# Kernel tuning notes

Hardware: AMD Instinct MI355X
Metric: run time of the kernel (lower is better)

## Reference

```python
import jax, jax.numpy as jnp
import numpy as np

N, E = 100000, 1600000
IN_C, HID, OUT_C, EDGE_D, GRAPH_D = 32, 32, 8, 16, 16

def _lin_w(key, fan_in, fan_out):
    return jax.random.normal(key, (fan_in, fan_out), dtype=jnp.float32) * (1.0 / np.sqrt(fan_in))

def setup_inputs() -> dict:
    key = jax.random.key(0)
    ks = jax.random.split(key, 12)
    return {
        "x": jax.random.uniform(ks[0], (N, IN_C), dtype=jnp.float32),
        "edge_attr": jax.random.uniform(ks[1], (E, EDGE_D), dtype=jnp.float32),
        "graph_attr": jax.random.uniform(ks[2], (1, GRAPH_D), dtype=jnp.float32),
        "edge_index": jax.random.randint(ks[3], (2, E), 0, N, dtype=jnp.int32),
        "batch": jnp.zeros((N,), dtype=jnp.int32),
        "W_node": _lin_w(ks[4], IN_C, HID),
        "b_node": jnp.zeros((HID,), jnp.float32),
        "W_graph": _lin_w(ks[5], GRAPH_D, GRAPH_D),
        "b_graph": jnp.zeros((GRAPH_D,), jnp.float32),
        "W_edge_agg": _lin_w(ks[6], 2 * HID + EDGE_D + GRAPH_D, EDGE_D),
        "b_edge_agg": jnp.zeros((EDGE_D,), jnp.float32),
        "W_node_agg": _lin_w(ks[7], EDGE_D + HID + GRAPH_D, HID),
        "b_node_agg": jnp.zeros((HID,), jnp.float32),
        "W_sage_l": _lin_w(ks[8], HID, OUT_C),
        "b_sage_l": jnp.zeros((OUT_C,), jnp.float32),
        "W_sage_r": _lin_w(ks[9], HID, OUT_C),
    }

def _seg_mean(vals, idx, num_segments):
    # scatter-mean: sum per segment / count (count clamped to 1 for empty segments)
    sums = jax.ops.segment_sum(vals, idx, num_segments=num_segments)
    cnt = jax.ops.segment_sum(jnp.ones((vals.shape[0],), vals.dtype), idx, num_segments=num_segments)
    return sums / jnp.maximum(cnt, 1.0)[:, None]

def reference(x, edge_attr, graph_attr, edge_index, batch,
              W_node, b_node, W_graph, b_graph,
              W_edge_agg, b_edge_agg, W_node_agg, b_node_agg,
              W_sage_l, b_sage_l, W_sage_r):
    n = x.shape[0]
    row, col = edge_index[0], edge_index[1]
    # node / graph embeddings (plain linear, no activation)
    h_i = x @ W_node + b_node                       # [N, HID]
    h_G = graph_attr @ W_graph + b_graph            # [1, GRAPH_D]
    h_G_e = jnp.broadcast_to(h_G, (row.shape[0], h_G.shape[1]))
    # edge aggregator: gather both endpoints, concat, linear, relu
    edge_in = jnp.concatenate([h_i[row], h_i[col], edge_attr, h_G_e], axis=-1)  # [E, 96]
    h_edge_agg = jax.nn.relu(edge_in @ W_edge_agg + b_edge_agg)                 # [E, EDGE_D]
    # per-node mean of edges whose source == node (replaces O(N*E) python loop)
    m_N = _seg_mean(h_edge_agg, row, n)             # [N, EDGE_D]
    # node aggregator
    h_G_n = jnp.broadcast_to(h_G, (n, h_G.shape[1]))
    h_i2 = jax.nn.relu(jnp.concatenate([h_i, m_N, h_G_n], axis=-1) @ W_node_agg + b_node_agg)
    # SAGEConv (mean aggr): out = lin_l(mean_{j->i} x_j) + lin_r(x_i)
    agg = _seg_mean(h_i2[row], col, n)
    h_nodes = agg @ W_sage_l + b_sage_l + h_i2 @ W_sage_r  # [N, OUT_C]
    # global mean pool over batch assignment (single graph here)
    pooled = _seg_mean(h_nodes, batch, 1)           # [1, OUT_C]
    return jax.nn.log_softmax(pooled, axis=1)
```

## Files before the change

kernel.cpp:

```cpp
#include <hip/hip_runtime.h>
#include <hip/hip_fp16.h>
#include <hip/hip_fp8.h>

#define HID 32
#define IN_C 32
#define EDGE_D 16
#define GRAPH_D 16
#define OUT_C 8
#define STRIDE 48
#define SLOT_B 32

__device__ __forceinline__ unsigned char f32_to_fp8(float f) {
    __hip_fp8_e4m3 v(f);
    return (unsigned char)v.__x;
}
__device__ __forceinline__ float fp8_to_f32(unsigned char b) {
    __hip_fp8_e4m3 v;
    v.__x = (__hip_fp8_storage_t)b;
    return (float)v;
}

__global__ void __launch_bounds__(256)
k_node_emb(const float* __restrict__ x,
           const float* __restrict__ W,
           const float* __restrict__ b,
           const float* __restrict__ graph_attr,
           const float* __restrict__ W_graph,
           const float* __restrict__ b_graph,
           const float* __restrict__ W_edge_agg,
           const float* __restrict__ b_edge_agg,
           const float* __restrict__ W_node_agg,
           const float* __restrict__ b_node_agg,
           float* __restrict__ bias_edge,
           float* __restrict__ bias_node,
           int* __restrict__ zero_base, int zero_count,
           __half* __restrict__ An,
           unsigned char* __restrict__ Pr,
           unsigned char* __restrict__ Pc, int n) {
    __shared__ float hG[GRAPH_D];
    int t = threadIdx.x;
    for (int idx = blockIdx.x * blockDim.x + t; idx < zero_count;
         idx += gridDim.x * blockDim.x)
        zero_base[idx] = 0;

    if (blockIdx.x == 0 && t < GRAPH_D) {
        float acc = b_graph[t];
        for (int d = 0; d < GRAPH_D; d++)
            acc += graph_attr[d] * W_graph[d * GRAPH_D + t];
        hG[t] = acc;
    }
    __syncthreads();
    if (blockIdx.x == 0) {
        if (t < EDGE_D) {
            float acc = b_edge_agg[t];
            for (int d = 0; d < GRAPH_D; d++)
                acc += hG[d] * W_edge_agg[(2 * HID + EDGE_D + d) * EDGE_D + t];
            bias_edge[t] = acc;
        }
        if (t < HID) {
            float acc = b_node_agg[t];
            for (int d = 0; d < GRAPH_D; d++)
                acc += hG[d] * W_node_agg[(HID + EDGE_D + d) * HID + t];
            bias_node[t] = acc;
        }
    }

    int i = blockIdx.x * blockDim.x + t;
    if (i >= n) return;
    float in[IN_C];
    const float4* xr = (const float4*)(x + (size_t)i * IN_C);
#pragma unroll
    for (int q = 0; q < IN_C / 4; q++) {
        float4 v = xr[q];
        in[4 * q + 0] = v.x; in[4 * q + 1] = v.y;
        in[4 * q + 2] = v.z; in[4 * q + 3] = v.w;
    }
    float acc[HID];
#pragma unroll
    for (int j = 0; j < HID; j++) acc[j] = b[j];
#pragma unroll
    for (int k = 0; k < IN_C; k++) {
        float a = in[k];
#pragma unroll
        for (int j = 0; j < HID; j++) acc[j] += a * W[k * HID + j];
    }

    {
        float pr[EDGE_D], pc[EDGE_D];
#pragma unroll
        for (int j = 0; j < EDGE_D; j++) { pr[j] = 0.f; pc[j] = 0.f; }
#pragma unroll
        for (int k = 0; k < HID; k++) {
            float a = acc[k];
#pragma unroll
            for (int j = 0; j < EDGE_D; j++) {
                pr[j] += a * W_edge_agg[k * EDGE_D + j];
                pc[j] += a * W_edge_agg[(HID + k) * EDGE_D + j];
            }
        }
        unsigned char pb[EDGE_D];
#pragma unroll
        for (int j = 0; j < EDGE_D; j++) pb[j] = f32_to_fp8(pr[j]);
        *(uint4*)(Pr + (size_t)i * EDGE_D) = *(const uint4*)pb;
#pragma unroll
        for (int j = 0; j < EDGE_D; j++) pb[j] = f32_to_fp8(pc[j]);
        *(uint4*)(Pc + (size_t)i * EDGE_D) = *(const uint4*)pb;
    }

    {
        float an[HID];
#pragma unroll
        for (int j = 0; j < HID; j++) an[j] = 0.f;
#pragma unroll
        for (int k = 0; k < HID; k++) {
            float a = acc[k];
#pragma unroll
            for (int j = 0; j < HID; j++) an[j] += a * W_node_agg[k * HID + j];
        }
        float4 packed[4];
        __half2* ph = (__half2*)packed;
#pragma unroll
        for (int j = 0; j < 16; j++)
            ph[j] = __floats2half2_rn(an[2 * j], an[2 * j + 1]);
        float4* dst = (float4*)(An + (size_t)i * HID);
#pragma unroll
        for (int q = 0; q < 4; q++) dst[q] = packed[q];
    }
}

__global__ void __launch_bounds__(256)
k_edge_place(const int* __restrict__ ei,
             const unsigned char* __restrict__ Pr,
             const unsigned char* __restrict__ Pc,
             const float* __restrict__ ea,
             const float* __restrict__ We,
             const float* __restrict__ biasE,
             int* __restrict__ cur_row,
             int* __restrict__ cur_col,
             unsigned char* __restrict__ he_bucket, int E) {
    int e = blockIdx.x * blockDim.x + threadIdx.x;
    if (e >= E) return;
    int r = ei[e];
    int c = ei[E + e];

    uint4 g = *(const uint4*)(Pr + (size_t)r * EDGE_D);
    uint4 q = *(const uint4*)(Pc + (size_t)c * EDGE_D);
    float eav[EDGE_D];
    {
        const float4* er = (const float4*)(ea + (size_t)e * EDGE_D);
#pragma unroll
        for (int k = 0; k < 4; k++) {
            float4 v = er[k];
            eav[4 * k + 0] = v.x; eav[4 * k + 1] = v.y;
            eav[4 * k + 2] = v.z; eav[4 * k + 3] = v.w;
        }
    }
    int pr = atomicAdd(cur_row + r, 1);
    atomicAdd(cur_col + c, 1);

    float acc[EDGE_D];
    {
        const unsigned char* gb = (const unsigned char*)&g;
        const unsigned char* qb = (const unsigned char*)&q;
#pragma unroll
        for (int j = 0; j < EDGE_D; j++)
            acc[j] = biasE[j] + fp8_to_f32(gb[j]) + fp8_to_f32(qb[j]);
    }
#pragma unroll
    for (int k = 0; k < EDGE_D; k++) {
        float a = eav[k];
#pragma unroll
        for (int j = 0; j < EDGE_D; j++)
            acc[j] += a * We[(2 * HID + k) * EDGE_D + j];
    }

    if (pr < STRIDE) {
        unsigned char hb[16];
#pragma unroll
        for (int j = 0; j < EDGE_D; j++)
            hb[j] = f32_to_fp8(fmaxf(acc[j], 0.f));
        uint4 w0 = *(const uint4*)hb;
        uint4 w1; w1.x = (unsigned int)c; w1.y = 0; w1.z = 0; w1.w = 0;
        unsigned char* dst = he_bucket + ((size_t)r * STRIDE + pr) * SLOT_B;
        *(uint4*)dst = w0;
        *(uint4*)(dst + 16) = w1;
    }
}

#define RNODES 128
__global__ void __launch_bounds__(256)
k_reduce(const __half* __restrict__ An,
         const unsigned char* __restrict__ he_bucket,
         const int* __restrict__ cur_row,
         const int* __restrict__ cur_col,
         const int* __restrict__ batch,
         const float* __restrict__ Wna,
         const float* __restrict__ biasN,
         float* __restrict__ Vg,
         float* __restrict__ Wg,
         float* __restrict__ ncnt, int n) {
    __shared__ float ms_s[RNODES][EDGE_D + 1];
    __shared__ float s_s[RNODES];
    __shared__ int cnt_s[RNODES];
    __shared__ float h2_s[RNODES][HID + 1];
    __shared__ float sv_s[RNODES];
    __shared__ float vq[8][HID];
    __shared__ float wq[8][HID];
    __shared__ float redc[2];
    int tid = threadIdx.x;
    int g = tid >> 4;
    int l = tid & 15;
    int base = blockIdx.x * RNODES;

    if (tid < RNODES)
        cnt_s[tid] = (base + tid < n) ? cur_row[base + tid] : 0;
    __syncthreads();

    for (int iter = 0; iter < RNODES / 16; iter++) {
        int node = base + iter * 16 + g;
        int cnt = cnt_s[iter * 16 + g];
        int d = cnt < STRIDE ? cnt : STRIDE;
        float inv = 1.0f / fmaxf((float)cnt, 1.0f);
        float a16[EDGE_D];
#pragma unroll
        for (int j = 0; j < EDGE_D; j++) a16[j] = 0.f;
        float sw = 0.f;
        const unsigned char* bb = he_bucket + (size_t)node * STRIDE * SLOT_B;
        for (int t = l; t < d; t += 16) {
            uint4 q0 = *(const uint4*)(bb + (size_t)t * SLOT_B);
            int col = *(const int*)(bb + (size_t)t * SLOT_B + 16);
            int ic = cur_col[col];
            sw += 1.0f / fmaxf((float)ic, 1.0f);
            const unsigned char* qb = (const unsigned char*)&q0;
#pragma unroll
            for (int j = 0; j < EDGE_D; j++)
                a16[j] += fp8_to_f32(qb[j]);
        }
#pragma unroll
        for (int m = 8; m >= 1; m >>= 1) {
#pragma unroll
            for (int k = 0; k < m; k++) {
                float send = (l & m) ? a16[k] : a16[k + m];
                float recv = __shfl_xor(send, m, 16);
                float keep = (l & m) ? a16[k + m] : a16[k];
                a16[k] = keep + recv;
            }
        }
#pragma unroll
        for (int m = 1; m <= 8; m <<= 1) sw += __shfl_xor(sw, m, 16);
        ms_s[iter * 16 + g][l] = a16[0] * inv;
        if (l == 0) s_s[iter * 16 + g] = sw;
    }
    __syncthreads();

    int i = base + tid;
    float cc = 0.f;
    if (tid < RNODES) {
        float h2[HID];
        float sv = 0.f;
        if (i < n) {
            float4 t4[4];
            const float4* arow = (const float4*)(An + (size_t)i * HID);
#pragma unroll
            for (int q = 0; q < 4; q++) t4[q] = arow[q];
            const __half2* hp = (const __half2*)t4;
#pragma unroll
            for (int j = 0; j < 16; j++) {
                float2 f = __half22float2(hp[j]);
                h2[2 * j]     = f.x + biasN[2 * j];
                h2[2 * j + 1] = f.y + biasN[2 * j + 1];
            }
#pragma unroll
            for (int k = 0; k < EDGE_D; k++) {
                float a = ms_s[tid][k];
#pragma unroll
                for (int j = 0; j < HID; j++)
                    h2[j] += a * Wna[(HID + k) * HID + j];
            }
#pragma unroll
            for (int j = 0; j < HID; j++) h2[j] = fmaxf(h2[j], 0.f);
            if (batch[i] == 0) { cc = 1.f; sv = s_s[tid]; }
            else {
#pragma unroll
                for (int j = 0; j < HID; j++) h2[j] = 0.f;
            }
        } else {
#pragma unroll
            for (int j = 0; j < HID; j++) h2[j] = 0.f;
        }
#pragma unroll
        for (int j = 0; j < HID; j++) h2_s[tid][j] = h2[j];
        sv_s[tid] = sv;
    }
    __syncthreads();

    {
        int ch = tid & 31;
        int q  = tid >> 5;
        float vsum = 0.f, wsum = 0.f;
        int nb = q * 16;
#pragma unroll
        for (int t2 = 0; t2 < 16; t2++) {
            float hval = h2_s[nb + t2][ch];
            float sval = sv_s[nb + t2];
            vsum += sval * hval;
            wsum += hval;
        }
        vq[q][ch] = vsum;
        wq[q][ch] = wsum;
    }
#pragma unroll
    for (int off = 32; off > 0; off >>= 1) cc += __shfl_down(cc, off, 64);
    if ((tid & 63) == 0 && tid < RNODES) redc[tid >> 6] = cc;
    __syncthreads();
    if (tid < HID) {
        float v = 0.f;
#pragma unroll
        for (int q = 0; q < 8; q++) v += vq[q][tid];
        atomicAdd(Vg + tid, v);
    } else if (tid < 2 * HID) {
        int j = tid - HID;
        float w = 0.f;
#pragma unroll
        for (int q = 0; q < 8; q++) w += wq[q][j];
        atomicAdd(Wg + j, w);
    } else if (tid == 2 * HID) {
        atomicAdd(ncnt, redc[0] + redc[1]);
    }
}

__global__ void k_final(const float* __restrict__ Vg,
                        const float* __restrict__ Wg,
                        const float* __restrict__ ncnt,
                        const float* __restrict__ Wsl,
                        const float* __restrict__ Wsr,
                        const float* __restrict__ bsl,
                        float* __restrict__ out) {
    if (threadIdx.x == 0 && blockIdx.x == 0) {
        float c = fmaxf(ncnt[0], 1.0f);
        float p[OUT_C];
        float m = -1e30f;
#pragma unroll
        for (int j = 0; j < OUT_C; j++) p[j] = 0.f;
        for (int k = 0; k < HID; k++) {
            float v = Vg[k], w = Wg[k];
#pragma unroll
            for (int j = 0; j < OUT_C; j++)
                p[j] += v * Wsl[k * OUT_C + j] + w * Wsr[k * OUT_C + j];
        }
#pragma unroll
        for (int j = 0; j < OUT_C; j++) {
            p[j] = p[j] / c + bsl[j];
            m = fmaxf(m, p[j]);
        }
        float s = 0.f;
#pragma unroll
        for (int j = 0; j < OUT_C; j++) s += expf(p[j] - m);
        float l = logf(s);
#pragma unroll
        for (int j = 0; j < OUT_C; j++) out[j] = p[j] - m - l;
    }
}

extern "C" void kernel_launch(void* const* d_in, const int* in_sizes, int n_in,
                              void* d_out, int out_size, void* d_ws, size_t ws_size,
                              hipStream_t stream) {
    const float* x          = (const float*)d_in[0];
    const float* edge_attr  = (const float*)d_in[1];
    const float* graph_attr = (const float*)d_in[2];
    const int*   edge_index = (const int*)d_in[3];
    const int*   batch      = (const int*)d_in[4];
    const float* W_node     = (const float*)d_in[5];
    const float* b_node     = (const float*)d_in[6];
    const float* W_graph    = (const float*)d_in[7];
    const float* b_graph    = (const float*)d_in[8];
    const float* W_edge_agg = (const float*)d_in[9];
    const float* b_edge_agg = (const float*)d_in[10];
    const float* W_node_agg = (const float*)d_in[11];
    const float* b_node_agg = (const float*)d_in[12];
    const float* W_sage_l   = (const float*)d_in[13];
    const float* b_sage_l   = (const float*)d_in[14];
    const float* W_sage_r   = (const float*)d_in[15];

    const int n = in_sizes[0] / IN_C;
    const int E = in_sizes[3] / 2;

    char* wsb = (char*)d_ws;
    int*  cur_row = (int*)wsb;
    int*  cur_col = cur_row + n;
    float* Vg     = (float*)(cur_col + n);
    float* Wg     = Vg + HID;
    float* ncnt   = Wg + HID;
    int   zero_count = 2 * n + 80;
    size_t off = (size_t)zero_count * 4;
    unsigned char* he_bucket = (unsigned char*)(wsb + off);
    off += (size_t)n * STRIDE * SLOT_B;
    __half* An   = (__half*)(wsb + off); off += (size_t)n * HID * 2;
    float* biasE = (float*)(wsb + off);  off += 16 * 4;
    float* biasN = (float*)(wsb + off);  off += HID * 4;
    unsigned char* Pr = (unsigned char*)(wsb + off); off += (size_t)n * EDGE_D;
    unsigned char* Pc = (unsigned char*)(wsb + off); off += (size_t)n * EDGE_D;

    k_node_emb<<<(n + 255) / 256, 256, 0, stream>>>(x, W_node, b_node,
                                                    graph_attr, W_graph, b_graph,
                                                    W_edge_agg, b_edge_agg,
                                                    W_node_agg, b_node_agg,
                                                    biasE, biasN,
                                                    cur_row, zero_count, An,
                                                    Pr, Pc, n);

    k_edge_place<<<(E + 255) / 256, 256, 0, stream>>>(edge_index, Pr, Pc, edge_attr,
                                                      W_edge_agg, biasE,
                                                      cur_row, cur_col,
                                                      he_bucket, E);

    k_reduce<<<(n + RNODES - 1) / RNODES, 256, 0, stream>>>(An, he_bucket,
                                                            cur_row, cur_col,
                                                            batch, W_node_agg,
                                                            biasN, Vg, Wg, ncnt, n);

    k_final<<<1, 64, 0, stream>>>(Vg, Wg, ncnt, W_sage_l, W_sage_r,
                                  b_sage_l, (float*)d_out);
}
```

Before: 503.1 us.

## Split reduce kernel into batched bucket reduce and full-occupancy node aggregation

The fused reduce kernel is split in two. The first kernel issues the bucket loads for all 8 node groups per slot round, so more memory requests are in flight and the cur_col gathers overlap. It writes per-node edge means as fp16 and the inverse-count sums to global scratch. The second kernel runs the node aggregation with all 256 threads active, where previously only 128 of 256 were, at the cost of an extra launch and an extra global round trip for the intermediates.

```diff
diff --git a/kernel.cpp b/kernel.cpp
--- a/kernel.cpp
+++ b/kernel.cpp
@@ -187,75 +187,108 @@
     }
 }
 
-#define RNODES 128
 __global__ void __launch_bounds__(256)
-k_reduce(const __half* __restrict__ An,
-         const unsigned char* __restrict__ he_bucket,
-         const int* __restrict__ cur_row,
-         const int* __restrict__ cur_col,
-         const int* __restrict__ batch,
-         const float* __restrict__ Wna,
-         const float* __restrict__ biasN,
-         float* __restrict__ Vg,
-         float* __restrict__ Wg,
-         float* __restrict__ ncnt, int n) {
-    __shared__ float ms_s[RNODES][EDGE_D + 1];
-    __shared__ float s_s[RNODES];
-    __shared__ int cnt_s[RNODES];
-    __shared__ float h2_s[RNODES][HID + 1];
-    __shared__ float sv_s[RNODES];
-    __shared__ float vq[8][HID];
-    __shared__ float wq[8][HID];
-    __shared__ float redc[2];
+k_bucket_reduce(const unsigned char* __restrict__ he_bucket,
+                const int* __restrict__ cur_row,
+                const int* __restrict__ cur_col,
+                __half* __restrict__ ms16,
+                float* __restrict__ s_arr, int n) {
+    __shared__ int cnt_s[128];
     int tid = threadIdx.x;
     int g = tid >> 4;
     int l = tid & 15;
-    int base = blockIdx.x * RNODES;
-
-    if (tid < RNODES)
+    int base = blockIdx.x * 128;
+
+    if (tid < 128)
         cnt_s[tid] = (base + tid < n) ? cur_row[base + tid] : 0;
     __syncthreads();
 
-    for (int iter = 0; iter < RNODES / 16; iter++) {
-        int node = base + iter * 16 + g;
-        int cnt = cnt_s[iter * 16 + g];
-        int d = cnt < STRIDE ? cnt : STRIDE;
+    float msum[8];
+    float sw[8];
+#pragma unroll
+    for (int it = 0; it < 8; it++) { msum[it] = 0.f; sw[it] = 0.f; }
+
+    for (int t0 = 0; t0 < STRIDE; t0 += 16) {
+        uint4 he[8]; int col[8]; bool act[8];
+#pragma unroll
+        for (int it = 0; it < 8; it++) {
+            int d = cnt_s[it * 16 + g]; if (d > STRIDE) d = STRIDE;
+            int slot = t0 + l;
+            act[it] = slot < d;
+            const unsigned char* p =
+                he_bucket + ((size_t)(base + it * 16 + g) * STRIDE + slot) * SLOT_B;
+            if (act[it]) {
+                he[it] = *(const uint4*)p;
+                col[it] = *(const int*)(p + 16);
+            } else {
+                he[it].x = he[it].y = he[it].z = he[it].w = 0u;
+                col[it] = 0;
+            }
+        }
+        float inv_[8];
+#pragma unroll
+        for (int it = 0; it < 8; it++) {
+            float ic = 1.f;
+            if (act[it]) ic = (float)cur_col[col[it]];
+            inv_[it] = act[it] ? 1.0f / fmaxf(ic, 1.0f) : 0.f;
+        }
+#pragma unroll
+        for (int it = 0; it < 8; it++) sw[it] += inv_[it];
+#pragma unroll
+        for (int it = 0; it < 8; it++) {
+            if (cnt_s[it * 16 + g] > t0) {
+                float a16[EDGE_D];
+                const unsigned char* qb = (const unsigned char*)&he[it];
+#pragma unroll
+                for (int j = 0; j < EDGE_D; j++) a16[j] = fp8_to_f32(qb[j]);
+#pragma unroll
+                for (int m = 8; m >= 1; m >>= 1) {
+#pragma unroll
+                    for (int k = 0; k < m; k++) {
+                        float send = (l & m) ? a16[k] : a16[k + m];
+                        float recv = __shfl_xor(send, m, 16);
+                        float keep = (l & m) ? a16[k + m] : a16[k];
+                        a16[k] = keep + recv;
+                    }
+                }
+                msum[it] += a16[0];
+            }
+        }
+    }
+
+#pragma unroll
+    for (int it = 0; it < 8; it++) {
+        int node = base + it * 16 + g;
+        int cnt = cnt_s[it * 16 + g];
         float inv = 1.0f / fmaxf((float)cnt, 1.0f);
-        float a16[EDGE_D];
-#pragma unroll
-        for (int j = 0; j < EDGE_D; j++) a16[j] = 0.f;
-        float sw = 0.f;
-        const unsigned char* bb = he_bucket + (size_t)node * STRIDE * SLOT_B;
-        for (int t = l; t < d; t += 16) {
-            uint4 q0 = *(const uint4*)(bb + (size_t)t * SLOT_B);
-            int col = *(const int*)(bb + (size_t)t * SLOT_B + 16);
-            int ic = cur_col[col];
-            sw += 1.0f / fmaxf((float)ic, 1.0f);
-            const unsigned char* qb = (const unsigned char*)&q0;
-#pragma unroll
-            for (int j = 0; j < EDGE_D; j++)
-                a16[j] += fp8_to_f32(qb[j]);
-        }
-#pragma unroll
-        for (int m = 8; m >= 1; m >>= 1) {
-#pragma unroll
-            for (int k = 0; k < m; k++) {
-                float send = (l & m) ? a16[k] : a16[k + m];
-                float recv = __shfl_xor(send, m, 16);
-                float keep = (l & m) ? a16[k + m] : a16[k];
-                a16[k] = keep + recv;
-            }
-        }
-#pragma unroll
-        for (int m = 1; m <= 8; m <<= 1) sw += __shfl_xor(sw, m, 16);
-        ms_s[iter * 16 + g][l] = a16[0] * inv;
-        if (l == 0) s_s[iter * 16 + g] = sw;
-    }
-    __syncthreads();
-
-    int i = base + tid;
+        if (node < n)
+            ms16[(size_t)node * EDGE_D + l] = __float2half(msum[it] * inv);
+        float v = sw[it];
+#pragma unroll
+        for (int m = 1; m <= 8; m <<= 1) v += __shfl_xor(v, m, 16);
+        if (l == 0 && node < n) s_arr[node] = v;
+    }
+}
+
+__global__ void __launch_bounds__(256)
+k_node_agg(const __half* __restrict__ An,
+           const __half* __restrict__ ms16,
+           const float* __restrict__ s_arr,
+           const int* __restrict__ batch,
+           const float* __restrict__ Wna,
+           const float* __restrict__ biasN,
+           float* __restrict__ Vg,
+           float* __restrict__ Wg,
+           float* __restrict__ ncnt, int n) {
+    __shared__ float h2_s[256][HID + 1];
+    __shared__ float sv_s[256];
+    __shared__ float vq[8][HID];
+    __shared__ float wq[8][HID];
+    __shared__ float redc[4];
+    int tid = threadIdx.x;
+    int i = blockIdx.x * 256 + tid;
     float cc = 0.f;
-    if (tid < RNODES) {
+    {
         float h2[HID];
         float sv = 0.f;
         if (i < n) {
@@ -270,16 +303,28 @@
                 h2[2 * j]     = f.x + biasN[2 * j];
                 h2[2 * j + 1] = f.y + biasN[2 * j + 1];
             }
+            float ms[EDGE_D];
+            {
+                float4 m4[2];
+                const float4* mrow = (const float4*)(ms16 + (size_t)i * EDGE_D);
+                m4[0] = mrow[0]; m4[1] = mrow[1];
+                const __half2* mp = (const __half2*)m4;
+#pragma unroll
+                for (int j = 0; j < 8; j++) {
+                    float2 f = __half22float2(mp[j]);
+                    ms[2 * j] = f.x; ms[2 * j + 1] = f.y;
+                }
+            }
 #pragma unroll
             for (int k = 0; k < EDGE_D; k++) {
-                float a = ms_s[tid][k];
+                float a = ms[k];
 #pragma unroll
                 for (int j = 0; j < HID; j++)
                     h2[j] += a * Wna[(HID + k) * HID + j];
             }
 #pragma unroll
             for (int j = 0; j < HID; j++) h2[j] = fmaxf(h2[j], 0.f);
-            if (batch[i] == 0) { cc = 1.f; sv = s_s[tid]; }
+            if (batch[i] == 0) { cc = 1.f; sv = s_arr[i]; }
             else {
 #pragma unroll
                 for (int j = 0; j < HID; j++) h2[j] = 0.f;
@@ -298,12 +343,11 @@
         int ch = tid & 31;
         int q  = tid >> 5;
         float vsum = 0.f, wsum = 0.f;
-        int nb = q * 16;
-#pragma unroll
-        for (int t2 = 0; t2 < 16; t2++) {
+        int nb = q * 32;
+#pragma unroll
+        for (int t2 = 0; t2 < 32; t2++) {
             float hval = h2_s[nb + t2][ch];
-            float sval = sv_s[nb + t2];
-            vsum += sval * hval;
+            vsum += sv_s[nb + t2] * hval;
             wsum += hval;
         }
         vq[q][ch] = vsum;
@@ -311,7 +355,7 @@
     }
 #pragma unroll
     for (int off = 32; off > 0; off >>= 1) cc += __shfl_down(cc, off, 64);
-    if ((tid & 63) == 0 && tid < RNODES) redc[tid >> 6] = cc;
+    if ((tid & 63) == 0) redc[tid >> 6] = cc;
     __syncthreads();
     if (tid < HID) {
         float v = 0.f;
@@ -325,7 +369,7 @@
         for (int q = 0; q < 8; q++) w += wq[q][j];
         atomicAdd(Wg + j, w);
     } else if (tid == 2 * HID) {
-        atomicAdd(ncnt, redc[0] + redc[1]);
+        atomicAdd(ncnt, redc[0] + redc[1] + redc[2] + redc[3]);
     }
 }
 
@@ -400,6 +444,8 @@
     float* biasN = (float*)(wsb + off);  off += HID * 4;
     unsigned char* Pr = (unsigned char*)(wsb + off); off += (size_t)n * EDGE_D;
     unsigned char* Pc = (unsigned char*)(wsb + off); off += (size_t)n * EDGE_D;
+    __half* ms16 = (__half*)(wsb + off); off += (size_t)n * EDGE_D * 2;
+    float* s_arr = (float*)(wsb + off);  off += (size_t)n * 4;
 
     k_node_emb<<<(n + 255) / 256, 256, 0, stream>>>(x, W_node, b_node,
                                                     graph_attr, W_graph, b_graph,
@@ -414,10 +460,12 @@
                                                       cur_row, cur_col,
                                                       he_bucket, E);
 
-    k_reduce<<<(n + RNODES - 1) / RNODES, 256, 0, stream>>>(An, he_bucket,
-                                                            cur_row, cur_col,
-                                                            batch, W_node_agg,
-                                                            biasN, Vg, Wg, ncnt, n);
+    k_bucket_reduce<<<(n + 127) / 128, 256, 0, stream>>>(he_bucket, cur_row,
+                                                         cur_col, ms16, s_arr, n);
+
+    k_node_agg<<<(n + 255) / 256, 256, 0, stream>>>(An, ms16, s_arr, batch,
+                                                    W_node_agg, biasN,
+                                                    Vg, Wg, ncnt, n);
 
     k_final<<<1, 64, 0, stream>>>(Vg, Wg, ncnt, W_sage_l, W_sage_r,
                                   b_sage_l, (float*)d_out);
```

Result: slower. 574.3 us (+14.2%).
